# Optimization experiments

Measured on AMD Instinct MI355X. Metric: run time of the kernel, lower is better.

Reference implementation:

```python
import jax, jax.numpy as jnp
import numpy as np

N, IN_CH, OUT_CH = 2, 16, 32
SPATIAL = (20, 20, 20, 20)
KER = (3, 3, 3, 3)


def setup_inputs() -> dict:
    key = jax.random.key(0)
    kx, kw = jax.random.split(key)
    x = jax.random.normal(kx, (N, IN_CH) + SPATIAL, dtype=jnp.float32)
    # kaiming-uniform-like init scale; exact init distribution irrelevant for correctness baseline
    fan_in = IN_CH * int(np.prod(KER))
    bound = float(np.sqrt(6.0 / fan_in))
    w = jax.random.uniform(kw, (IN_CH, OUT_CH) + KER, dtype=jnp.float32,
                           minval=-bound, maxval=bound)
    return {"x": x, "w": w}


def reference(x, w):
    # x: [n, in_ch, d1, d2, d3, d4]; w: [in_ch, out_ch, k1, k2, k3, k4]
    # valid 4D convolution (cross-correlation), stride 1 -- same math as the
    # torch as_strided im2col + tensordot, but expressed as a sum over the
    # (small, fixed) kernel offsets to avoid materializing the im2col tensor.
    kd = w.shape[2:]
    od = tuple(x.shape[2 + i] - kd[i] + 1 for i in range(4))  # output spatial dims
    out = jnp.zeros((x.shape[0], w.shape[1]) + od, dtype=x.dtype)
    for a in range(kd[0]):
        for b in range(kd[1]):
            for c in range(kd[2]):
                for d in range(kd[3]):
                    patch = x[:, :, a:a + od[0], b:b + od[1], c:c + od[2], d:d + od[3]]
                    out = out + jnp.einsum('ncijkl,co->noijkl', patch, w[:, :, a, b, c, d])
    return out
```

## Files before the change

kernel.cpp:

```cpp
#include <hip/hip_runtime.h>


typedef unsigned short ushort_t;
typedef __attribute__((ext_vector_type(8)))  __bf16 bf16x8;
typedef __attribute__((ext_vector_type(16))) float  f32x16;
typedef __attribute__((ext_vector_type(4)))  unsigned int uint4v;

__device__ __forceinline__ ushort_t f2bf(float f) {
    union { float f; unsigned int u; } v; v.f = f;
    unsigned int r = v.u + 0x7FFFu + ((v.u >> 16) & 1u);
    return (ushort_t)(r >> 16);
}

__global__ __launch_bounds__(256) void prep_w(const float* __restrict__ w,
                                              ushort_t* __restrict__ wt) {
    int s = blockIdx.x * 256 + threadIdx.x;
    if (s < 41472) {
        int ic = s / 2592, rem = s % 2592;
        int oc = rem / 81, tap = rem % 81;
        wt[tap * 512 + oc * 16 + ic] = f2bf(w[s]);
    }
}

__global__ __launch_bounds__(256, 2) void conv4d_fused(
    const float* __restrict__ x, const ushort_t* __restrict__ wt,
    float* __restrict__ out)
{
    __shared__ ushort_t lx[2][6400];
    __shared__ float edgebuf[4][3][2][16];

    const int wgid = blockIdx.x;
    const int tile_ = (wgid & 7) * 81 + (wgid >> 3);
    const int n = tile_ / 324;
    const int rem_ = tile_ - n * 324;
    const int j = rem_ / 18, i = rem_ % 18;

    const int t = threadIdx.x;
    const int lane = t & 63, wv = t >> 6;
    const int col = lane & 31, ic8 = lane >> 5;

    int sp[3]; int cb[3];
    #pragma unroll
    for (int m = 0; m < 3; ++m) {
        sp[m] = (3 * wv + m) * 32 + col;
        const int spc = sp[m] > 359 ? 359 : sp[m];
        cb[m] = spc * 32 + ic8 * 16;
    }

    f32x16 acc[3][3];
    #pragma unroll
    for (int d = 0; d < 3; ++d)
        #pragma unroll
        for (int m = 0; m < 3; ++m)
            #pragma unroll
            for (int r = 0; r < 16; ++r) acc[d][m][r] = 0.0f;

    const float* xn = x + (size_t)n * 2560000;
    const bool stg = (t < 200);
    const int p0 = 2 * t;
    const int wlog = 64 * t;
    const int wphys = wlog ^ (((wlog >> 7) & 7) << 4);

    float2 val[16];

    if (stg) {
        const float* xr = xn + (size_t)i * 8000 + (size_t)j * 400 + p0;
        #pragma unroll
        for (int ic = 0; ic < 16; ++ic)
            val[ic] = *(const float2*)(xr + (size_t)ic * 160000);
        char* base = (char*)lx[0];
        uint4v c0, c1, c2, c3;
        #pragma unroll
        for (int m = 0; m < 4; ++m) {
            c0[m] = (unsigned)f2bf(val[2*m].x)     | ((unsigned)f2bf(val[2*m+1].x) << 16);
            c1[m] = (unsigned)f2bf(val[2*m+8].x)   | ((unsigned)f2bf(val[2*m+9].x) << 16);
            c2[m] = (unsigned)f2bf(val[2*m].y)     | ((unsigned)f2bf(val[2*m+1].y) << 16);
            c3[m] = (unsigned)f2bf(val[2*m+8].y)   | ((unsigned)f2bf(val[2*m+9].y) << 16);
        }
        *(uint4v*)(base + (wphys ^ 0))  = c0;
        *(uint4v*)(base + (wphys ^ 16)) = c1;
        *(uint4v*)(base + (wphys ^ 32)) = c2;
        *(uint4v*)(base + (wphys ^ 48)) = c3;
    }

    int cur = 0;
    for (int ab = 0; ab < 9; ++ab) {
        __syncthreads();

        bf16x8 af[9];
        const ushort_t* wtb = wt + (size_t)(ab * 9) * 512 + col * 16 + ic8 * 8;
        #pragma unroll
        for (int cd = 0; cd < 9; ++cd)
            af[cd] = *(const bf16x8*)(wtb + cd * 512);

        if (ab < 8 && stg) {
            const int a = (ab + 1) / 3, b = (ab + 1) % 3;
            const float* xr = xn + (size_t)(i + a) * 8000 + (size_t)(j + b) * 400 + p0;
            #pragma unroll
            for (int ic = 0; ic < 16; ++ic)
                val[ic] = *(const float2*)(xr + (size_t)ic * 160000);
        }

        const char* lbase = (const char*)lx[cur];
        #pragma unroll
        for (int c = 0; c < 3; ++c) {
            #pragma unroll
            for (int m = 0; m < 3; ++m) {
                const int lg = cb[m] + c * 640;
                const int ph = lg ^ (((lg >> 7) & 7) << 4);
                bf16x8 bv = *(const bf16x8*)(lbase + ph);
                acc[0][m] = __builtin_amdgcn_mfma_f32_32x32x16_bf16(af[c*3+0], bv, acc[0][m], 0, 0, 0);
                acc[1][m] = __builtin_amdgcn_mfma_f32_32x32x16_bf16(af[c*3+1], bv, acc[1][m], 0, 0, 0);
                acc[2][m] = __builtin_amdgcn_mfma_f32_32x32x16_bf16(af[c*3+2], bv, acc[2][m], 0, 0, 0);
            }
        }

        if (ab < 8) {
            if (stg) {
                char* base = (char*)lx[cur ^ 1];
                uint4v c0, c1, c2, c3;
                #pragma unroll
                for (int m = 0; m < 4; ++m) {
                    c0[m] = (unsigned)f2bf(val[2*m].x)   | ((unsigned)f2bf(val[2*m+1].x) << 16);
                    c1[m] = (unsigned)f2bf(val[2*m+8].x) | ((unsigned)f2bf(val[2*m+9].x) << 16);
                    c2[m] = (unsigned)f2bf(val[2*m].y)   | ((unsigned)f2bf(val[2*m+1].y) << 16);
                    c3[m] = (unsigned)f2bf(val[2*m+8].y) | ((unsigned)f2bf(val[2*m+9].y) << 16);
                }
                *(uint4v*)(base + (wphys ^ 0))  = c0;
                *(uint4v*)(base + (wphys ^ 16)) = c1;
                *(uint4v*)(base + (wphys ^ 32)) = c2;
                *(uint4v*)(base + (wphys ^ 48)) = c3;
            }
            cur ^= 1;
        }
    }

    if (col == 0) {
        #pragma unroll
        for (int r = 0; r < 16; ++r) {
            edgebuf[wv][0][ic8][r] = acc[1][0][r];
            edgebuf[wv][1][ic8][r] = acc[2][0][r];
        }
    } else if (col == 1) {
        #pragma unroll
        for (int r = 0; r < 16; ++r)
            edgebuf[wv][2][ic8][r] = acc[2][0][r];
    }
    __syncthreads();
    const int nw = wv < 3 ? wv + 1 : 3;

    bool valm[3]; float* po[3];
    float* outn = out + (size_t)n * 3359232 + (size_t)i * 5832 + (size_t)j * 324
                      + (size_t)ic8 * 419904;
    #pragma unroll
    for (int m = 0; m < 3; ++m) {
        const int s = sp[m];
        const int k = s / 20, ls = s % 20;
        valm[m] = (ls <= 17) && (s <= 357);
        po[m] = outn + k * 18 + ls;
    }
    const int src1 = (lane & 32) | ((col + 1) & 31);
    const int src2 = (lane & 32) | ((col + 2) & 31);

    #pragma unroll
    for (int r = 0; r < 16; ++r) {
        const float e1  = edgebuf[nw][0][ic8][r];
        const float e2a = edgebuf[nw][1][ic8][r];
        const float e2b = edgebuf[nw][2][ic8][r];
        float t1[4], t2[4];
        #pragma unroll
        for (int m = 0; m < 3; ++m) {
            t1[m] = __shfl(acc[1][m][r], src1, 64);
            t2[m] = __shfl(acc[2][m][r], src2, 64);
        }
        t1[3] = e1;
        t2[3] = (col == 30) ? e2a : e2b;
        const int offr = ((r & 3) + 8 * (r >> 2)) * 104976;
        #pragma unroll
        for (int m = 0; m < 3; ++m) {
            const float v1 = (col == 31) ? t1[m + 1] : t1[m];
            const float v2 = (col >= 30) ? t2[m + 1] : t2[m];
            const float res = acc[0][m][r] + v1 + v2;
            if (valm[m]) po[m][offr] = res;
        }
    }
}

extern "C" void kernel_launch(void* const* d_in, const int* in_sizes, int n_in,
                              void* d_out, int out_size, void* d_ws, size_t ws_size,
                              hipStream_t stream) {
    const float* x = (const float*)d_in[0];
    const float* w = (const float*)d_in[1];
    float* out = (float*)d_out;

    ushort_t* wt = (ushort_t*)d_ws;

    prep_w<<<dim3(162), 256, 0, stream>>>(w, wt);
    conv4d_fused<<<dim3(648), 256, 0, stream>>>(x, wt, out);
}
```

Before: 48.79 us.

## Stage weights in LDS via async global_load_lds and split input prefetch in halves

Weight fragments for each (a,b) tap group are now copied asynchronously into a double-buffered LDS array with global_load_lds, prefetched one iteration ahead, instead of being loaded from global into registers every iteration. The next input slice prefetch is split into two halves of eight channels, with the first half converted and stored between MFMA groups, to lower register pressure and overlap loads with compute. This adds LDS usage (about 18 KB more), which may reduce occupancy. It also depends on async LDS loads completing before the next barrier without an explicit vmcnt wait.

```diff
diff --git a/kernel.cpp b/kernel.cpp
--- a/kernel.cpp
+++ b/kernel.cpp
@@ -10,6 +10,12 @@
     union { float f; unsigned int u; } v; v.f = f;
     unsigned int r = v.u + 0x7FFFu + ((v.u >> 16) & 1u);
     return (ushort_t)(r >> 16);
+}
+
+__device__ __forceinline__ void gload16(const ushort_t* g, ushort_t* l) {
+    __builtin_amdgcn_global_load_lds(
+        (const __attribute__((address_space(1))) unsigned int*)g,
+        (__attribute__((address_space(3))) unsigned int*)l, 16, 0, 0);
 }
 
 __global__ __launch_bounds__(256) void prep_w(const float* __restrict__ w,
@@ -27,6 +33,7 @@
     float* __restrict__ out)
 {
     __shared__ ushort_t lx[2][6400];
+    __shared__ ushort_t lwt[2][4608];
     __shared__ float edgebuf[4][3][2][16];
 
     const int wgid = blockIdx.x;
@@ -61,21 +68,28 @@
     const int wlog = 64 * t;
     const int wphys = wlog ^ (((wlog >> 7) & 7) << 4);
 
-    float2 val[16];
-
+    const int aoff = col * 32 + ic8 * 16;
+
+    {
+        const ushort_t* g = wt;
+        gload16(g + t * 8,        lwt[0] + (wv << 9));
+        gload16(g + 2048 + t * 8, lwt[0] + 2048 + (wv << 9));
+        if (t < 64) gload16(g + 4096 + t * 8, lwt[0] + 4096);
+    }
     if (stg) {
         const float* xr = xn + (size_t)i * 8000 + (size_t)j * 400 + p0;
+        float2 v[16];
         #pragma unroll
         for (int ic = 0; ic < 16; ++ic)
-            val[ic] = *(const float2*)(xr + (size_t)ic * 160000);
+            v[ic] = *(const float2*)(xr + (size_t)ic * 160000);
         char* base = (char*)lx[0];
         uint4v c0, c1, c2, c3;
         #pragma unroll
         for (int m = 0; m < 4; ++m) {
-            c0[m] = (unsigned)f2bf(val[2*m].x)     | ((unsigned)f2bf(val[2*m+1].x) << 16);
-            c1[m] = (unsigned)f2bf(val[2*m+8].x)   | ((unsigned)f2bf(val[2*m+9].x) << 16);
-            c2[m] = (unsigned)f2bf(val[2*m].y)     | ((unsigned)f2bf(val[2*m+1].y) << 16);
-            c3[m] = (unsigned)f2bf(val[2*m+8].y)   | ((unsigned)f2bf(val[2*m+9].y) << 16);
+            c0[m] = (unsigned)f2bf(v[2*m].x)   | ((unsigned)f2bf(v[2*m+1].x) << 16);
+            c1[m] = (unsigned)f2bf(v[2*m+8].x) | ((unsigned)f2bf(v[2*m+9].x) << 16);
+            c2[m] = (unsigned)f2bf(v[2*m].y)   | ((unsigned)f2bf(v[2*m+1].y) << 16);
+            c3[m] = (unsigned)f2bf(v[2*m+8].y) | ((unsigned)f2bf(v[2*m+9].y) << 16);
         }
         *(uint4v*)(base + (wphys ^ 0))  = c0;
         *(uint4v*)(base + (wphys ^ 16)) = c1;
@@ -87,48 +101,86 @@
     for (int ab = 0; ab < 9; ++ab) {
         __syncthreads();
 
-        bf16x8 af[9];
-        const ushort_t* wtb = wt + (size_t)(ab * 9) * 512 + col * 16 + ic8 * 8;
-        #pragma unroll
-        for (int cd = 0; cd < 9; ++cd)
-            af[cd] = *(const bf16x8*)(wtb + cd * 512);
-
+        const int nxt = ab + 1;
+        if (ab < 8) {
+            const ushort_t* g = wt + (size_t)nxt * 4608;
+            ushort_t* l = lwt[nxt & 1];
+            gload16(g + t * 8,        l + (wv << 9));
+            gload16(g + 2048 + t * 8, l + 2048 + (wv << 9));
+            if (t < 64) gload16(g + 4096 + t * 8, l + 4096);
+        }
+
+        const float* xr = (ab < 8)
+            ? xn + (size_t)(i + nxt / 3) * 8000 + (size_t)(j + nxt % 3) * 400 + p0
+            : nullptr;
+
+        float2 v1[8];
         if (ab < 8 && stg) {
-            const int a = (ab + 1) / 3, b = (ab + 1) % 3;
-            const float* xr = xn + (size_t)(i + a) * 8000 + (size_t)(j + b) * 400 + p0;
-            #pragma unroll
-            for (int ic = 0; ic < 16; ++ic)
-                val[ic] = *(const float2*)(xr + (size_t)ic * 160000);
+            #pragma unroll
+            for (int ic = 0; ic < 8; ++ic)
+                v1[ic] = *(const float2*)(xr + (size_t)ic * 160000);
         }
 
         const char* lbase = (const char*)lx[cur];
-        #pragma unroll
-        for (int c = 0; c < 3; ++c) {
+        const char* wbase = (const char*)lwt[ab & 1];
+
+        {
+            bf16x8 af0 = *(const bf16x8*)(wbase + 0 * 1024 + aoff);
+            bf16x8 af1 = *(const bf16x8*)(wbase + 1 * 1024 + aoff);
+            bf16x8 af2 = *(const bf16x8*)(wbase + 2 * 1024 + aoff);
+            #pragma unroll
+            for (int m = 0; m < 3; ++m) {
+                const int lg = cb[m];
+                const int ph = lg ^ (((lg >> 7) & 7) << 4);
+                bf16x8 bv = *(const bf16x8*)(lbase + ph);
+                acc[0][m] = __builtin_amdgcn_mfma_f32_32x32x16_bf16(af0, bv, acc[0][m], 0, 0, 0);
+                acc[1][m] = __builtin_amdgcn_mfma_f32_32x32x16_bf16(af1, bv, acc[1][m], 0, 0, 0);
+                acc[2][m] = __builtin_amdgcn_mfma_f32_32x32x16_bf16(af2, bv, acc[2][m], 0, 0, 0);
+            }
+        }
+
+        float2 v2[8];
+        if (ab < 8 && stg) {
+            char* base = (char*)lx[cur ^ 1];
+            uint4v c0, c2;
+            #pragma unroll
+            for (int m = 0; m < 4; ++m) {
+                c0[m] = (unsigned)f2bf(v1[2*m].x) | ((unsigned)f2bf(v1[2*m+1].x) << 16);
+                c2[m] = (unsigned)f2bf(v1[2*m].y) | ((unsigned)f2bf(v1[2*m+1].y) << 16);
+            }
+            *(uint4v*)(base + (wphys ^ 0))  = c0;
+            *(uint4v*)(base + (wphys ^ 32)) = c2;
+            #pragma unroll
+            for (int ic = 0; ic < 8; ++ic)
+                v2[ic] = *(const float2*)(xr + (size_t)(ic + 8) * 160000);
+        }
+
+        #pragma unroll
+        for (int c = 1; c < 3; ++c) {
+            bf16x8 af0 = *(const bf16x8*)(wbase + (c * 3 + 0) * 1024 + aoff);
+            bf16x8 af1 = *(const bf16x8*)(wbase + (c * 3 + 1) * 1024 + aoff);
+            bf16x8 af2 = *(const bf16x8*)(wbase + (c * 3 + 2) * 1024 + aoff);
             #pragma unroll
             for (int m = 0; m < 3; ++m) {
                 const int lg = cb[m] + c * 640;
                 const int ph = lg ^ (((lg >> 7) & 7) << 4);
                 bf16x8 bv = *(const bf16x8*)(lbase + ph);
-                acc[0][m] = __builtin_amdgcn_mfma_f32_32x32x16_bf16(af[c*3+0], bv, acc[0][m], 0, 0, 0);
-                acc[1][m] = __builtin_amdgcn_mfma_f32_32x32x16_bf16(af[c*3+1], bv, acc[1][m], 0, 0, 0);
-                acc[2][m] = __builtin_amdgcn_mfma_f32_32x32x16_bf16(af[c*3+2], bv, acc[2][m], 0, 0, 0);
+                acc[0][m] = __builtin_amdgcn_mfma_f32_32x32x16_bf16(af0, bv, acc[0][m], 0, 0, 0);
+                acc[1][m] = __builtin_amdgcn_mfma_f32_32x32x16_bf16(af1, bv, acc[1][m], 0, 0, 0);
+                acc[2][m] = __builtin_amdgcn_mfma_f32_32x32x16_bf16(af2, bv, acc[2][m], 0, 0, 0);
             }
         }
 
         if (ab < 8) {
             if (stg) {
                 char* base = (char*)lx[cur ^ 1];
-                uint4v c0, c1, c2, c3;
+                uint4v c1, c3;
                 #pragma unroll
                 for (int m = 0; m < 4; ++m) {
-                    c0[m] = (unsigned)f2bf(val[2*m].x)   | ((unsigned)f2bf(val[2*m+1].x) << 16);
-                    c1[m] = (unsigned)f2bf(val[2*m+8].x) | ((unsigned)f2bf(val[2*m+9].x) << 16);
-                    c2[m] = (unsigned)f2bf(val[2*m].y)   | ((unsigned)f2bf(val[2*m+1].y) << 16);
-                    c3[m] = (unsigned)f2bf(val[2*m+8].y) | ((unsigned)f2bf(val[2*m+9].y) << 16);
+                    c1[m] = (unsigned)f2bf(v2[2*m].x) | ((unsigned)f2bf(v2[2*m+1].x) << 16);
+                    c3[m] = (unsigned)f2bf(v2[2*m].y) | ((unsigned)f2bf(v2[2*m+1].y) << 16);
                 }
-                *(uint4v*)(base + (wphys ^ 0))  = c0;
                 *(uint4v*)(base + (wphys ^ 16)) = c1;
-                *(uint4v*)(base + (wphys ^ 32)) = c2;
                 *(uint4v*)(base + (wphys ^ 48)) = c3;
             }
             cur ^= 1;
@@ -178,9 +230,9 @@
         const int offr = ((r & 3) + 8 * (r >> 2)) * 104976;
         #pragma unroll
         for (int m = 0; m < 3; ++m) {
-            const float v1 = (col == 31) ? t1[m + 1] : t1[m];
-            const float v2 = (col >= 30) ? t2[m + 1] : t2[m];
-            const float res = acc[0][m][r] + v1 + v2;
+            const float v1m = (col == 31) ? t1[m + 1] : t1[m];
+            const float v2m = (col >= 30) ? t2[m + 1] : t2[m];
+            const float res = acc[0][m][r] + v1m + v2m;
             if (valm[m]) po[m][offr] = res;
         }
     }
```

Result: no change. 49.57 us (+1.6%).
